# Kernel tuning notes

Measured on AMD Instinct MI355X. Metric: run time of the kernel, lower is better.

## Reference

```python
import jax, jax.numpy as jnp
import numpy as np

B, N, F, U, S = 64, 4096, 2, 16, 2


def setup_inputs() -> dict:
    key = jax.random.key(0)
    ks = jax.random.split(key, 7)
    inputs = jax.random.normal(ks[0], (B, F * N), dtype=jnp.float32)
    state = jax.random.normal(ks[1], (B, U * N), dtype=jnp.float32)

    def random_walk(k):
        a = jax.random.uniform(k, (N, N), dtype=jnp.float32)
        return a / jnp.sum(a, axis=1, keepdims=True)  # row-stochastic like D^-1 A

    support0 = random_walk(ks[2])
    support1 = random_walk(ks[3])
    kshape = ((F + U) * S, U)
    scale = jnp.float32(1.0 / np.sqrt(kshape[0]))
    r_kernel = jax.random.normal(ks[4], kshape, dtype=jnp.float32) * scale
    u_kernel = jax.random.normal(ks[5], kshape, dtype=jnp.float32) * scale
    c_kernel = jax.random.normal(ks[6], kshape, dtype=jnp.float32) * scale
    return {"inputs": inputs, "state": state, "support0": support0,
            "support1": support1, "r_kernel": r_kernel, "u_kernel": u_kernel,
            "c_kernel": c_kernel}


def _diffuse(x, supports):
    # x: (B, C, N); K.dot(x, support.T)[b,c,m] = sum_n x[b,c,n] * support[m,n]
    return jnp.concatenate([jnp.einsum('bcn,mn->bcm', x, s) for s in supports], axis=1)


def reference(inputs, state, support0, support1, r_kernel, u_kernel, c_kernel):
    supports = (support0, support1)
    feats = inputs.reshape(B, F, N)
    prev = state.reshape(B, U, N)

    h = _diffuse(feats, supports).transpose(0, 2, 1)   # (B, N, S*F)
    st = _diffuse(prev, supports).transpose(0, 2, 1)   # (B, N, S*U)
    hs = jnp.concatenate([h, st], axis=-1)             # (B, N, S*(F+U))

    r = jax.nn.sigmoid(hs @ r_kernel)                  # (B, N, U)
    u = jax.nn.sigmoid(hs @ u_kernel)                  # (B, N, U)

    prev_t = prev.transpose(0, 2, 1)                   # (B, N, U)
    r_prev = (r * prev_t).transpose(0, 2, 1)           # (B, U, N)
    c_state = _diffuse(r_prev, supports).transpose(0, 2, 1)  # (B, N, S*U)
    c = jnp.tanh(jnp.concatenate([h, c_state], axis=-1) @ c_kernel)  # (B, N, U)

    z = u * prev_t + (1.0 - u) * c                     # (B, N, U)
    # original: activation=None -> linear, then K.reshape(output, (-1, units*num_nodes))
    return z.reshape(B, U * N)
```

## Files before the change

kernel.cpp:

```cpp
#include <hip/hip_runtime.h>
#include <cstdint>

#define KDIM 4096
#define NNODE 4096
#define KSPLIT 2
#define TSTEPS 128
#define THALF (TSTEPS / KSPLIT)

typedef __bf16 bf16x8 __attribute__((ext_vector_type(8)));
typedef float floatx4 __attribute__((ext_vector_type(4)));

__device__ __forceinline__ uint16_t f2b(float f) {
  union { float f; uint32_t u; } v; v.f = f;
  uint32_t u = v.u;
  return (uint16_t)((u + 0x7FFFu + ((u >> 16) & 1u)) >> 16);
}
__device__ __forceinline__ float b2f(uint16_t h) {
  union { uint32_t u; float f; } v; v.u = ((uint32_t)h) << 16; return v.f;
}
__device__ __forceinline__ uint32_t pack2(float a, float b) {
  return (uint32_t)f2b(a) | ((uint32_t)f2b(b) << 16);
}


__global__ __launch_bounds__(256) void cvt_supports(
    const float* __restrict__ s0, const float* __restrict__ s1,
    uint16_t* __restrict__ d0, uint16_t* __restrict__ d1) {
  const float* src = blockIdx.z ? s1 : s0;
  uint16_t* dst = blockIdx.z ? d1 : d0;
  const int c16 = blockIdx.x, kb = blockIdx.y;
  const int col_in = threadIdx.x >> 4, k8 = threadIdx.x & 15;
  const int col = c16 * 16 + col_in;
  const int k = kb * 128 + k8 * 8;
  const float* p = src + (size_t)col * KDIM + k;
  float4 v0 = *(const float4*)p;
  float4 v1 = *(const float4*)(p + 4);
  uint4 o;
  o.x = pack2(v0.x, v0.y); o.y = pack2(v0.z, v0.w);
  o.z = pack2(v1.x, v1.y); o.w = pack2(v1.z, v1.w);
  size_t off = ((size_t)(c16 * 128 + kb * 4 + (k8 >> 2))) * 512 +
               (size_t)((k8 & 3) * 16 + col_in) * 8;
  *(uint4*)(dst + off) = o;
}

__global__ __launch_bounds__(256) void pack_x1(
    const float* __restrict__ inp, const float* __restrict__ st,
    uint16_t* __restrict__ X1) {
  const int r16 = blockIdx.x, kb = blockIdx.y;
  const int row_in = threadIdx.x >> 4, k8 = threadIdx.x & 15;
  const int row = r16 * 16 + row_in;
  const int k = kb * 128 + k8 * 8;
  int b = row / 18, c = row - b * 18;
  const float* p = (c < 2) ? (inp + (size_t)b * 8192 + (size_t)c * 4096 + k)
                           : (st + (size_t)b * 65536 + (size_t)(c - 2) * 4096 + k);
  float4 v0 = *(const float4*)p;
  float4 v1 = *(const float4*)(p + 4);
  uint4 o;
  o.x = pack2(v0.x, v0.y); o.y = pack2(v0.z, v0.w);
  o.z = pack2(v1.x, v1.y); o.w = pack2(v1.z, v1.w);
  size_t off = ((size_t)(r16 * 128 + kb * 4 + (k8 >> 2))) * 512 +
               (size_t)((k8 & 3) * 16 + row_in) * 8;
  *(uint4*)(X1 + off) = o;
}

__device__ __forceinline__ void gl_lds16(const uint16_t* g, uint16_t* l) {
  __builtin_amdgcn_global_load_lds(
      (const __attribute__((address_space(1))) uint32_t*)g,
      (__attribute__((address_space(3))) uint32_t*)l, 16, 0, 0);
}

template <int MODE>
__global__ __launch_bounds__(256, 2) void gemm_frag(
    const uint16_t* __restrict__ Af, const uint16_t* __restrict__ S0f,
    const uint16_t* __restrict__ S1f, uint16_t* __restrict__ D) {
  constexpr int CPB = (MODE == 1) ? 18 : 16;
  constexpr int OUTC = (MODE == 1) ? 36 : 32;
  constexpr size_t PSTRIDE = (size_t)64 * OUTC * NNODE;
  constexpr int NCH = THALF;

  __shared__ uint16_t sAB[3][24][512];

  const int lane = threadIdx.x & 63, wave = threadIdx.x >> 6;
  const int wr = wave >> 1, wc = wave & 1;
  const int s = blockIdx.z & 1, ks = blockIdx.z >> 1;
  const uint16_t* __restrict__ Bf = s ? S1f : S0f;
  const int yF = blockIdx.y * 8;
  const int xF = blockIdx.x * 16;
  const int tBeg = ks * THALF;

  const uint16_t* Gp[6];
#pragma unroll
  for (int i = 0; i < 6; ++i) {
    int fid = wave * 6 + i;
    bool isA = fid < 8;
    int fr = isA ? (yF + fid) : (xF + fid - 8);
    const uint16_t* base = isA ? Af : Bf;
    Gp[i] = base + ((size_t)fr * 128 + tBeg) * 512 + (size_t)lane * 8;
  }

  floatx4 acc[4][8];
#pragma unroll
  for (int i = 0; i < 4; ++i)
#pragma unroll
    for (int j = 0; j < 8; ++j) acc[i][j] = (floatx4){0.f, 0.f, 0.f, 0.f};

  auto STAGE = [&](int bi, int c) {
    uint16_t* l = &sAB[bi][wave * 6][0];
    const size_t off = (size_t)c * 512;
#pragma unroll
    for (int i = 0; i < 6; ++i)
      gl_lds16(Gp[i] + off, l + (size_t)i * 512);
  };

  auto LDREG = [&](int bi, bf16x8* a, bf16x8* b) {
    const uint16_t* base = &sAB[bi][0][lane * 8];
#pragma unroll
    for (int rt = 0; rt < 4; ++rt)
      a[rt] = *(const bf16x8*)(base + (size_t)(wr * 4 + rt) * 512);
#pragma unroll
    for (int ct = 0; ct < 8; ++ct)
      b[ct] = *(const bf16x8*)(base + (size_t)(8 + wc * 8 + ct) * 512);
  };

  auto MFMA32 = [&](bf16x8* a, bf16x8* b) {
    __builtin_amdgcn_s_setprio(1);
#pragma unroll
    for (int rt = 0; rt < 4; ++rt)
#pragma unroll
      for (int ct = 0; ct < 8; ++ct)
        acc[rt][ct] = __builtin_amdgcn_mfma_f32_16x16x32_bf16(
            a[rt], b[ct], acc[rt][ct], 0, 0, 0);
    __builtin_amdgcn_s_setprio(0);
  };

  STAGE(0, 0);
  STAGE(1, 1);
  asm volatile("s_waitcnt vmcnt(6)" ::: "memory");
  __builtin_amdgcn_sched_barrier(0);
  __builtin_amdgcn_s_barrier();
  __builtin_amdgcn_sched_barrier(0);
  bf16x8 aA[4], bA[8], aB[4], bB[8];
  LDREG(0, aA, bA);

  int bN = 1, bS = 2;
#define GEMM_ITER(CC, CURA, CURB, NXTA, NXTB)                               \
  {                                                                         \
    int cl = (CC) + 2;                                                      \
    if (cl > NCH - 1) cl = NCH - 1;       \
    STAGE(bS, cl);                                                          \
    asm volatile("s_waitcnt vmcnt(6)" ::: "memory");                        \
    __builtin_amdgcn_sched_barrier(0);                                      \
    __builtin_amdgcn_s_barrier();                                           \
    __builtin_amdgcn_sched_barrier(0);                                      \
    LDREG(bN, NXTA, NXTB);                                                  \
    asm volatile("s_waitcnt lgkmcnt(12)" ::: "memory");                     \
    __builtin_amdgcn_sched_barrier(0);                                      \
    MFMA32(CURA, CURB);                                                     \
    __builtin_amdgcn_sched_barrier(0);                                      \
    bN = (bN == 2) ? 0 : bN + 1;                                            \
    bS = (bS == 2) ? 0 : bS + 1;                                            \
  }

  for (int c = 0; c < NCH; c += 2) {
    GEMM_ITER(c,     aA, bA, aB, bB)
    GEMM_ITER(c + 1, aB, bB, aA, bA)
  }
#undef GEMM_ITER

  uint16_t* Dp = D + (size_t)ks * PSTRIDE;
#pragma unroll
  for (int rt = 0; rt < 4; ++rt) {
#pragma unroll
    for (int r = 0; r < 4; ++r) {
      int rowg = yF * 16 + wr * 64 + rt * 16 + (lane >> 4) * 4 + r;
      int b = rowg / CPB, c = rowg - b * CPB;
      int jj;
      if (MODE == 1) jj = (c < 2) ? (2 * s + c) : (4 + 16 * s + (c - 2));
      else jj = 16 * s + c;
      uint16_t* drow = Dp + (size_t)(b * OUTC + jj) * NNODE;
#pragma unroll
      for (int ct = 0; ct < 8; ++ct) {
        int colg = xF * 16 + wc * 128 + ct * 16 + (lane & 15);
        drow[colg] = f2b(acc[rt][ct][r]);
      }
    }
  }
}

__global__ __launch_bounds__(256) void stage2(
    const uint16_t* __restrict__ P1, const float* __restrict__ state,
    const float* __restrict__ rk, const float* __restrict__ uk,
    uint16_t* __restrict__ X2f, float* __restrict__ U) {
  constexpr size_t PS = (size_t)64 * 36 * NNODE;
  __shared__ float s_rk[576], s_uk[576];
  __shared__ uint16_t s_x2[16 * 264];
  for (int i = threadIdx.x; i < 576; i += 256) { s_rk[i] = rk[i]; s_uk[i] = uk[i]; }
  __syncthreads();
  const int b = blockIdx.x >> 4, nb = blockIdx.x & 15;
  const int i = threadIdx.x;
  const int n = nb * 256 + i;
  float hs[36];
  const uint16_t* p = P1 + (size_t)b * 36 * NNODE + n;
#pragma unroll
  for (int j = 0; j < 36; ++j)
    hs[j] = b2f(p[(size_t)j * NNODE]) + b2f(p[PS + (size_t)j * NNODE]);
  float ar[16], au[16];
#pragma unroll
  for (int k = 0; k < 16; ++k) { ar[k] = 0.f; au[k] = 0.f; }
#pragma unroll
  for (int j = 0; j < 36; ++j) {
    float h = hs[j];
#pragma unroll
    for (int k = 0; k < 16; ++k) {
      ar[k] += h * s_rk[j * 16 + k];
      au[k] += h * s_uk[j * 16 + k];
    }
  }
  const float* sp = state + (size_t)b * 65536 + n;
#pragma unroll
  for (int k = 0; k < 16; ++k) {
    float r = 1.f / (1.f + __expf(-ar[k]));
    float uu = 1.f / (1.f + __expf(-au[k]));
    float prev = sp[(size_t)k * NNODE];
    s_x2[k * 264 + i] = f2b(r * prev);
    U[(size_t)(b * 16 + k) * NNODE + n] = uu;
  }
  __syncthreads();
  uint16_t* region = X2f + ((size_t)b * 128 + nb * 8) * 512;
#pragma unroll
  for (int rr = 0; rr < 2; ++rr) {
    int fid = rr * 256 + i;
    int kk = fid & 15, qq = (fid >> 4) & 3, tl = fid >> 6;
    uint4 v = *(const uint4*)&s_x2[kk * 264 + tl * 32 + qq * 8];
    *(uint4*)(region + (size_t)fid * 8) = v;
  }
}

__global__ __launch_bounds__(256) void stage4(
    const uint16_t* __restrict__ P1, const uint16_t* __restrict__ P3,
    const float* __restrict__ U, const float* __restrict__ state,
    const float* __restrict__ ck, float* __restrict__ out) {
  constexpr size_t PS1 = (size_t)64 * 36 * NNODE;
  constexpr size_t PS3 = (size_t)64 * 32 * NNODE;
  __shared__ float s_ck[576];
  for (int i = threadIdx.x; i < 576; i += 256) s_ck[i] = ck[i];
  __syncthreads();
  int idx = blockIdx.x * 256 + threadIdx.x;
  int b = idx >> 12, n = idx & 4095;
  float hv[36];
  const uint16_t* p1 = P1 + (size_t)b * 36 * NNODE + n;
#pragma unroll
  for (int j = 0; j < 4; ++j)
    hv[j] = b2f(p1[(size_t)j * NNODE]) + b2f(p1[PS1 + (size_t)j * NNODE]);
  const uint16_t* p3 = P3 + (size_t)b * 32 * NNODE + n;
#pragma unroll
  for (int j = 0; j < 32; ++j)
    hv[4 + j] = b2f(p3[(size_t)j * NNODE]) + b2f(p3[PS3 + (size_t)j * NNODE]);
  float ac[16];
#pragma unroll
  for (int k = 0; k < 16; ++k) ac[k] = 0.f;
#pragma unroll
  for (int j = 0; j < 36; ++j) {
    float h = hv[j];
#pragma unroll
    for (int k = 0; k < 16; ++k) ac[k] += h * s_ck[j * 16 + k];
  }
  const float* sp = state + (size_t)b * 65536 + n;
  const float* up = U + (size_t)b * 16 * NNODE + n;
  float z[16];
#pragma unroll
  for (int k = 0; k < 16; ++k) {
    float e = __expf(2.f * ac[k]);
    float c = 1.f - 2.f / (e + 1.f);
    float uu = up[(size_t)k * NNODE];
    float prev = sp[(size_t)k * NNODE];
    z[k] = uu * prev + (1.f - uu) * c;
  }
  float4* po = (float4*)(out + (size_t)b * 65536 + (size_t)n * 16);
#pragma unroll
  for (int k4 = 0; k4 < 4; ++k4)
    po[k4] = make_float4(z[k4 * 4], z[k4 * 4 + 1], z[k4 * 4 + 2], z[k4 * 4 + 3]);
}

extern "C" void kernel_launch(void* const* d_in, const int* in_sizes, int n_in,
                              void* d_out, int out_size, void* d_ws, size_t ws_size,
                              hipStream_t stream) {
  const float* inputs = (const float*)d_in[0];
  const float* state = (const float*)d_in[1];
  const float* s0 = (const float*)d_in[2];
  const float* s1 = (const float*)d_in[3];
  const float* rk = (const float*)d_in[4];
  const float* uk = (const float*)d_in[5];
  const float* ck = (const float*)d_in[6];
  float* out = (float*)d_out;
  char* ws = (char*)d_ws;

  uint16_t* S0f = (uint16_t*)(ws);
  uint16_t* S1f = (uint16_t*)(ws + 33554432);
  uint16_t* X1f = (uint16_t*)(ws + 67108864);
  uint16_t* X2f = (uint16_t*)(ws + 67108864);
  uint16_t* P1 = (uint16_t*)(ws + 76546048);
  float* U = (float*)(ws + 114294784);
  uint16_t* P3 = (uint16_t*)(ws + 131072000);

  cvt_supports<<<dim3(256, 32, 2), 256, 0, stream>>>(s0, s1, S0f, S1f);
  pack_x1<<<dim3(72, 32), 256, 0, stream>>>(inputs, state, X1f);
  gemm_frag<1><<<dim3(16, 9, 2 * KSPLIT), 256, 0, stream>>>(X1f, S0f, S1f, P1);
  stage2<<<1024, 256, 0, stream>>>(P1, state, rk, uk, X2f, U);
  gemm_frag<3><<<dim3(16, 8, 2 * KSPLIT), 256, 0, stream>>>(X2f, S0f, S1f, P3);
  stage4<<<1024, 256, 0, stream>>>(P1, P3, U, state, ck, out);
}
```

Measured before the change: 364.5 us.

## Drop split-K in diffusion GEMMs, use 512-thread blocks with larger tiles

Removes the two-way K split so each GEMM block walks the full reduction and writes a single bf16 partial, which lets stage2 and stage4 read one buffer instead of summing two. Blocks grow to 8 waves, tiles grow to 9 or 8 A-fragments by 16 B-fragments, and a 4-deep LDS ring buffer with 3-ahead prefetch replaces the 3-deep one. This is meant to cut partial-sum write and read traffic and raise operand reuse per block, at the cost of half as many blocks (256 per GEMM) and longer per-block loops, which may leave CUs underused.

```diff
diff --git a/kernel.cpp b/kernel.cpp
--- a/kernel.cpp
+++ b/kernel.cpp
@@ -3,9 +3,7 @@
 
 #define KDIM 4096
 #define NNODE 4096
-#define KSPLIT 2
 #define TSTEPS 128
-#define THALF (TSTEPS / KSPLIT)
 
 typedef __bf16 bf16x8 __attribute__((ext_vector_type(8)));
 typedef float floatx4 __attribute__((ext_vector_type(4)));
@@ -70,117 +68,134 @@
 }
 
 template <int MODE>
-__global__ __launch_bounds__(256, 2) void gemm_frag(
+__global__ __launch_bounds__(512, 2) void gemm_frag(
     const uint16_t* __restrict__ Af, const uint16_t* __restrict__ S0f,
     const uint16_t* __restrict__ S1f, uint16_t* __restrict__ D) {
-  constexpr int CPB = (MODE == 1) ? 18 : 16;
-  constexpr int OUTC = (MODE == 1) ? 36 : 32;
-  constexpr size_t PSTRIDE = (size_t)64 * OUTC * NNODE;
-  constexpr int NCH = THALF;
-
-  __shared__ uint16_t sAB[3][24][512];
+  constexpr int CPB   = (MODE == 1) ? 18 : 16;
+  constexpr int OUTC  = (MODE == 1) ? 36 : 32;
+  constexpr int MFR   = (MODE == 1) ? 9 : 8;
+  constexpr int WM    = (MODE == 1) ? 1 : 2;
+  constexpr int WN    = 8 / WM;
+  constexpr int AR    = MFR / WM;
+  constexpr int BR    = 16 / WN;
+  constexpr int NREAL = MFR + 16;
+  constexpr int SLOTS = (NREAL + 7) & ~7;
+  constexpr int LPW   = SLOTS / 8;
+  constexpr int NCH   = TSTEPS;
+
+  __shared__ uint16_t sAB[4][SLOTS][512];
 
   const int lane = threadIdx.x & 63, wave = threadIdx.x >> 6;
-  const int wr = wave >> 1, wc = wave & 1;
-  const int s = blockIdx.z & 1, ks = blockIdx.z >> 1;
+  const int wr = wave / WN, wc = wave % WN;
+  const int s = blockIdx.z;
   const uint16_t* __restrict__ Bf = s ? S1f : S0f;
-  const int yF = blockIdx.y * 8;
+  const int yF = blockIdx.y * MFR;
   const int xF = blockIdx.x * 16;
-  const int tBeg = ks * THALF;
-
-  const uint16_t* Gp[6];
-#pragma unroll
-  for (int i = 0; i < 6; ++i) {
-    int fid = wave * 6 + i;
-    bool isA = fid < 8;
-    int fr = isA ? (yF + fid) : (xF + fid - 8);
-    const uint16_t* base = isA ? Af : Bf;
-    Gp[i] = base + ((size_t)fr * 128 + tBeg) * 512 + (size_t)lane * 8;
-  }
-
-  floatx4 acc[4][8];
-#pragma unroll
-  for (int i = 0; i < 4; ++i)
-#pragma unroll
-    for (int j = 0; j < 8; ++j) acc[i][j] = (floatx4){0.f, 0.f, 0.f, 0.f};
+
+  const uint16_t* Gp[LPW];
+#pragma unroll
+  for (int i = 0; i < LPW; ++i) {
+    int sid = wave * LPW + i;
+    const uint16_t* base;
+    int fr;
+    if (sid < MFR)        { base = Af; fr = yF + sid; }
+    else if (sid < NREAL) { base = Bf; fr = xF + sid - MFR; }
+    else                  { base = Af; fr = yF; }
+    Gp[i] = base + (size_t)fr * (TSTEPS * 512) + (size_t)lane * 8;
+  }
+
+  floatx4 acc[AR][BR];
+#pragma unroll
+  for (int i = 0; i < AR; ++i)
+#pragma unroll
+    for (int j = 0; j < BR; ++j) acc[i][j] = (floatx4){0.f, 0.f, 0.f, 0.f};
 
   auto STAGE = [&](int bi, int c) {
-    uint16_t* l = &sAB[bi][wave * 6][0];
+    uint16_t* l = &sAB[bi][wave * LPW][0];
     const size_t off = (size_t)c * 512;
 #pragma unroll
-    for (int i = 0; i < 6; ++i)
+    for (int i = 0; i < LPW; ++i)
       gl_lds16(Gp[i] + off, l + (size_t)i * 512);
   };
 
   auto LDREG = [&](int bi, bf16x8* a, bf16x8* b) {
     const uint16_t* base = &sAB[bi][0][lane * 8];
 #pragma unroll
-    for (int rt = 0; rt < 4; ++rt)
-      a[rt] = *(const bf16x8*)(base + (size_t)(wr * 4 + rt) * 512);
-#pragma unroll
-    for (int ct = 0; ct < 8; ++ct)
-      b[ct] = *(const bf16x8*)(base + (size_t)(8 + wc * 8 + ct) * 512);
-  };
-
-  auto MFMA32 = [&](bf16x8* a, bf16x8* b) {
+    for (int rt = 0; rt < AR; ++rt)
+      a[rt] = *(const bf16x8*)(base + (size_t)(wr * AR + rt) * 512);
+#pragma unroll
+    for (int ct = 0; ct < BR; ++ct)
+      b[ct] = *(const bf16x8*)(base + (size_t)(MFR + wc * BR + ct) * 512);
+  };
+
+  auto MFMAALL = [&](bf16x8* a, bf16x8* b) {
     __builtin_amdgcn_s_setprio(1);
 #pragma unroll
-    for (int rt = 0; rt < 4; ++rt)
-#pragma unroll
-      for (int ct = 0; ct < 8; ++ct)
+    for (int rt = 0; rt < AR; ++rt)
+#pragma unroll
+      for (int ct = 0; ct < BR; ++ct)
         acc[rt][ct] = __builtin_amdgcn_mfma_f32_16x16x32_bf16(
             a[rt], b[ct], acc[rt][ct], 0, 0, 0);
     __builtin_amdgcn_s_setprio(0);
   };
 
+  auto waitVM = [&] {
+    if constexpr (MODE == 1) asm volatile("s_waitcnt vmcnt(8)" ::: "memory");
+    else                     asm volatile("s_waitcnt vmcnt(6)" ::: "memory");
+  };
+  auto waitLG = [&] {
+    if constexpr (MODE == 1) asm volatile("s_waitcnt lgkmcnt(11)" ::: "memory");
+    else                     asm volatile("s_waitcnt lgkmcnt(8)" ::: "memory");
+  };
+
   STAGE(0, 0);
   STAGE(1, 1);
-  asm volatile("s_waitcnt vmcnt(6)" ::: "memory");
+  STAGE(2, 2);
+  waitVM();
   __builtin_amdgcn_sched_barrier(0);
   __builtin_amdgcn_s_barrier();
   __builtin_amdgcn_sched_barrier(0);
-  bf16x8 aA[4], bA[8], aB[4], bB[8];
+  bf16x8 aA[AR], bA[BR], aB[AR], bB[BR];
   LDREG(0, aA, bA);
 
-  int bN = 1, bS = 2;
-#define GEMM_ITER(CC, CURA, CURB, NXTA, NXTB)                               \
+#define GITER(J, SB, RB, CA, CB, NA, NB)                                    \
   {                                                                         \
-    int cl = (CC) + 2;                                                      \
+    int cl = c0 + 3 + (J);                                                  \
     if (cl > NCH - 1) cl = NCH - 1;       \
-    STAGE(bS, cl);                                                          \
-    asm volatile("s_waitcnt vmcnt(6)" ::: "memory");                        \
+    STAGE((SB), cl);                                                        \
+    waitVM();                                                               \
     __builtin_amdgcn_sched_barrier(0);                                      \
     __builtin_amdgcn_s_barrier();                                           \
     __builtin_amdgcn_sched_barrier(0);                                      \
-    LDREG(bN, NXTA, NXTB);                                                  \
-    asm volatile("s_waitcnt lgkmcnt(12)" ::: "memory");                     \
+    LDREG((RB), NA, NB);                                                    \
+    waitLG();                                                               \
     __builtin_amdgcn_sched_barrier(0);                                      \
-    MFMA32(CURA, CURB);                                                     \
+    MFMAALL(CA, CB);                                                        \
     __builtin_amdgcn_sched_barrier(0);                                      \
-    bN = (bN == 2) ? 0 : bN + 1;                                            \
-    bS = (bS == 2) ? 0 : bS + 1;                                            \
-  }
-
-  for (int c = 0; c < NCH; c += 2) {
-    GEMM_ITER(c,     aA, bA, aB, bB)
-    GEMM_ITER(c + 1, aB, bB, aA, bA)
-  }
-#undef GEMM_ITER
-
-  uint16_t* Dp = D + (size_t)ks * PSTRIDE;
-#pragma unroll
-  for (int rt = 0; rt < 4; ++rt) {
+  }
+
+  for (int m = 0; m < NCH / 4; ++m) {
+    const int c0 = m * 4;
+    GITER(0, 3, 1, aA, bA, aB, bB)
+    GITER(1, 0, 2, aB, bB, aA, bA)
+    GITER(2, 1, 3, aA, bA, aB, bB)
+    GITER(3, 2, 0, aB, bB, aA, bA)
+  }
+#undef GITER
+
+#pragma unroll
+  for (int rt = 0; rt < AR; ++rt) {
 #pragma unroll
     for (int r = 0; r < 4; ++r) {
-      int rowg = yF * 16 + wr * 64 + rt * 16 + (lane >> 4) * 4 + r;
+      int rowg = (yF + wr * AR + rt) * 16 + (lane >> 4) * 4 + r;
       int b = rowg / CPB, c = rowg - b * CPB;
       int jj;
       if (MODE == 1) jj = (c < 2) ? (2 * s + c) : (4 + 16 * s + (c - 2));
       else jj = 16 * s + c;
-      uint16_t* drow = Dp + (size_t)(b * OUTC + jj) * NNODE;
-#pragma unroll
-      for (int ct = 0; ct < 8; ++ct) {
-        int colg = xF * 16 + wc * 128 + ct * 16 + (lane & 15);
+      uint16_t* drow = D + (size_t)(b * OUTC + jj) * NNODE;
+#pragma unroll
+      for (int ct = 0; ct < BR; ++ct) {
+        int colg = xF * 16 + (wc * BR + ct) * 16 + (lane & 15);
         drow[colg] = f2b(acc[rt][ct][r]);
       }
     }
@@ -191,7 +206,6 @@
     const uint16_t* __restrict__ P1, const float* __restrict__ state,
     const float* __restrict__ rk, const float* __restrict__ uk,
     uint16_t* __restrict__ X2f, float* __restrict__ U) {
-  constexpr size_t PS = (size_t)64 * 36 * NNODE;
   __shared__ float s_rk[576], s_uk[576];
   __shared__ uint16_t s_x2[16 * 264];
   for (int i = threadIdx.x; i < 576; i += 256) { s_rk[i] = rk[i]; s_uk[i] = uk[i]; }
@@ -203,7 +217,7 @@
   const uint16_t* p = P1 + (size_t)b * 36 * NNODE + n;
 #pragma unroll
   for (int j = 0; j < 36; ++j)
-    hs[j] = b2f(p[(size_t)j * NNODE]) + b2f(p[PS + (size_t)j * NNODE]);
+    hs[j] = b2f(p[(size_t)j * NNODE]);
   float ar[16], au[16];
 #pragma unroll
   for (int k = 0; k < 16; ++k) { ar[k] = 0.f; au[k] = 0.f; }
@@ -240,8 +254,6 @@
     const uint16_t* __restrict__ P1, const uint16_t* __restrict__ P3,
     const float* __restrict__ U, const float* __restrict__ state,
     const float* __restrict__ ck, float* __restrict__ out) {
-  constexpr size_t PS1 = (size_t)64 * 36 * NNODE;
-  constexpr size_t PS3 = (size_t)64 * 32 * NNODE;
   __shared__ float s_ck[576];
   for (int i = threadIdx.x; i < 576; i += 256) s_ck[i] = ck[i];
   __syncthreads();
@@ -251,11 +263,11 @@
   const uint16_t* p1 = P1 + (size_t)b * 36 * NNODE + n;
 #pragma unroll
   for (int j = 0; j < 4; ++j)
-    hv[j] = b2f(p1[(size_t)j * NNODE]) + b2f(p1[PS1 + (size_t)j * NNODE]);
+    hv[j] = b2f(p1[(size_t)j * NNODE]);
   const uint16_t* p3 = P3 + (size_t)b * 32 * NNODE + n;
 #pragma unroll
   for (int j = 0; j < 32; ++j)
-    hv[4 + j] = b2f(p3[(size_t)j * NNODE]) + b2f(p3[PS3 + (size_t)j * NNODE]);
+    hv[4 + j] = b2f(p3[(size_t)j * NNODE]);
   float ac[16];
 #pragma unroll
   for (int k = 0; k < 16; ++k) ac[k] = 0.f;
@@ -305,8 +317,8 @@
 
   cvt_supports<<<dim3(256, 32, 2), 256, 0, stream>>>(s0, s1, S0f, S1f);
   pack_x1<<<dim3(72, 32), 256, 0, stream>>>(inputs, state, X1f);
-  gemm_frag<1><<<dim3(16, 9, 2 * KSPLIT), 256, 0, stream>>>(X1f, S0f, S1f, P1);
+  gemm_frag<1><<<dim3(16, 8, 2), 512, 0, stream>>>(X1f, S0f, S1f, P1);
   stage2<<<1024, 256, 0, stream>>>(P1, state, rk, uk, X2f, U);
-  gemm_frag<3><<<dim3(16, 8, 2 * KSPLIT), 256, 0, stream>>>(X2f, S0f, S1f, P3);
+  gemm_frag<3><<<dim3(16, 8, 2), 512, 0, stream>>>(X2f, S0f, S1f, P3);
   stage4<<<1024, 256, 0, stream>>>(P1, P3, U, state, ck, out);
 }
```

Result: faster. 345.6 us (-5.2%).
